# Optimization experiments

Hardware: AMD Instinct MI355X
Metric: run time of the kernel (lower is better)

Reference implementation:

```python
import jax, jax.numpy as jnp
import numpy as np

K = 1.0          # Lorentz curvature (all three manifolds)
SQRTK = 1.0
EPS = 1e-8
RES_SCALE = 27.5 # LResNet scale inside blocks
PE_SCALE = 1.0   # LResNet scale for positional embedding add
PATCH = 14


def ldot(x, y):
    """Minkowski inner product over last axis."""
    return -x[..., 0] * y[..., 0] + jnp.sum(x[..., 1:] * y[..., 1:], axis=-1)


def add_time(s):
    """Lift space components s to the hyperboloid: x0 = sqrt(1/K + ||s||^2)."""
    t = jnp.sqrt(1.0 / K + jnp.sum(s * s, axis=-1, keepdims=True))
    return jnp.concatenate([t, s], axis=-1)


def lnormalize(z):
    """Project arbitrary vector back onto hyperboloid (<x,x>_L = -1/K)."""
    d = jnp.sqrt(jnp.clip(-ldot(z, z), EPS))[..., None]
    return z / (SQRTK * d)


def lresnet(x, y, scale):
    """Lorentzian residual: normalized weighted Euclidean sum (LResNet)."""
    return lnormalize(x + scale * y)


def llayernorm(x, g, b):
    """LorentzLayerNorm: LayerNorm on space components, recompute time."""
    s = x[..., 1:]
    mu = jnp.mean(s, axis=-1, keepdims=True)
    var = jnp.var(s, axis=-1, keepdims=True)
    return add_time((s - mu) / jnp.sqrt(var + 1e-5) * g + b)


def lgelu(x):
    """LorentzActivation(GELU): act on space components, recompute time."""
    return add_time(jax.nn.gelu(x[..., 1:]))


def lattention(x, wq, bq, wk, bk, wv, bv, wo, bo):
    """Lorentz multi-head full attention, trans_heads_concat=True.
    x: [B,N,D]; wq/wk/wv: [H,D,hc-1]; wo: [D,D-1]."""
    q = add_time(jnp.einsum('bnd,hde->bhne', x, wq) + bq[None, :, None, :])
    k = add_time(jnp.einsum('bnd,hde->bhne', x, wk) + bk[None, :, None, :])
    v = add_time(jnp.einsum('bnd,hde->bhne', x, wv) + bv[None, :, None, :])
    hc = q.shape[-1]
    # pairwise Minkowski inner products -> neg. squared Lorentz distance scores
    inner = (jnp.einsum('bhne,bhme->bhnm', q[..., 1:], k[..., 1:])
             - q[..., 0][..., None] * k[..., 0][..., None, :])
    scores = (2.0 / K + 2.0 * inner) / jnp.sqrt(jnp.asarray(hc, x.dtype))
    att = jax.nn.softmax(scores, axis=-1)
    m = jnp.einsum('bhnm,bhmc->bhnc', att, v)   # convex combo of hyperbolic pts
    out = lnormalize(m)                          # Lorentzian centroid, [B,H,N,hc]
    B, H, N, C = out.shape
    cat = out.transpose(0, 2, 1, 3).reshape(B, N, H * C)
    return add_time(cat @ wo + bo)


def _forward(x, patch_W, patch_b, pe,
             ln1_g, ln1_b, ln2_g, ln2_b,
             Wq, bq, Wk, bk, Wv, bv, Wo, bo,
             mlp_W1, mlp_b1, mlp_W2, mlp_b2,
             mlr_a, mlr_z):
    B = x.shape[0]
    xi = x.transpose(0, 2, 3, 1)            # [B,H,W,3]
    xh = add_time(xi)                       # projx(pad(x,(1,0))) -> [B,H,W,4]
    _, Hh, Wh, Ch = xh.shape
    hp, wp = Hh // PATCH, Wh // PATCH
    patches = (xh.reshape(B, hp, PATCH, wp, PATCH, Ch)
                 .transpose(0, 1, 3, 2, 4, 5)
                 .reshape(B, hp * wp, PATCH * PATCH * Ch))
    h = add_time(patches @ patch_W + patch_b)   # Lorentz patch embed, [B,N,D]
    h = lresnet(h, pe, PE_SCALE)                # add positional embedding

    def body(h, p):
        (g1, b1, g2, b2, wq, bq_, wk, bk_, wv, bv_, wo, bo_,
         w1, b1m, w2, b2m) = p
        h = llayernorm(h, g1, b1)
        a = lattention(h, wq, bq_, wk, bk_, wv, bv_, wo, bo_)
        h = lresnet(h, a, RES_SCALE)
        m = llayernorm(h, g2, b2)
        m = add_time(m @ w1 + b1m)              # LorentzLinear 1
        m = lgelu(m)
        m = add_time(m @ w2 + b2m)              # LorentzLinear 2 (dropout=0)
        h = lresnet(h, m, RES_SCALE)
        return h, None

    h, _ = jax.lax.scan(body, h,
                        (ln1_g, ln1_b, ln2_g, ln2_b, Wq, bq, Wk, bk, Wv, bv,
                         Wo, bo, mlp_W1, mlp_b1, mlp_W2, mlp_b2))

    emb = lnormalize(jnp.mean(h, axis=1))       # lorentzian_centroid, [B,D]

    # LorentzMLR classifier
    zn = jnp.sqrt(jnp.sum(mlr_z * mlr_z, axis=-1) + EPS)
    wt = jnp.sinh(SQRTK * mlr_a) * zn                 # [C]
    ws = jnp.cosh(SQRTK * mlr_a)[:, None] * mlr_z     # [C,D-1]
    beta = jnp.sqrt(jnp.clip(jnp.sum(ws * ws, -1) - wt * wt, EPS))
    alpha = -emb[:, 0:1] * wt[None, :] + emb[:, 1:] @ ws.T  # [B,C]
    logits = beta * jnp.arcsinh(SQRTK * alpha / beta) / SQRTK
    return logits


def setup_inputs() -> dict:
    key = jax.random.key(0)
    ks = jax.random.split(key, 16)
    B, IMG, P, H, HC, L, C = 32, 224, 14, 6, 64, 12, 1000
    D = H * HC
    N = (IMG // P) ** 2
    MH = 4 * D
    s = 0.02
    f = jax.random.normal
    return dict(
        x=f(ks[0], (B, 3, IMG, IMG), jnp.float32),
        patch_W=f(ks[1], (P * P * 4, D - 1)) * s,
        patch_b=jnp.zeros((D - 1,)),
        pe=add_time(f(ks[2], (1, N, D - 1)) * s),
        ln1_g=jnp.ones((L, D - 1)), ln1_b=jnp.zeros((L, D - 1)),
        ln2_g=jnp.ones((L, D - 1)), ln2_b=jnp.zeros((L, D - 1)),
        Wq=f(ks[3], (L, H, D, HC - 1)) * s, bq=jnp.zeros((L, H, HC - 1)),
        Wk=f(ks[4], (L, H, D, HC - 1)) * s, bk=jnp.zeros((L, H, HC - 1)),
        Wv=f(ks[5], (L, H, D, HC - 1)) * s, bv=jnp.zeros((L, H, HC - 1)),
        Wo=f(ks[6], (L, D, D - 1)) * s, bo=jnp.zeros((L, D - 1)),
        mlp_W1=f(ks[7], (L, D, MH - 1)) * s, mlp_b1=jnp.zeros((L, MH - 1)),
        mlp_W2=f(ks[8], (L, MH, D - 1)) * s, mlp_b2=jnp.zeros((L, D - 1)),
        mlr_a=f(ks[9], (C,)) * s,
        mlr_z=f(ks[10], (C, D - 1)) * s,
    )


def reference(x, patch_W, patch_b, pe,
              ln1_g, ln1_b, ln2_g, ln2_b,
              Wq, bq, Wk, bk, Wv, bv, Wo, bo,
              mlp_W1, mlp_b1, mlp_W2, mlp_b2,
              mlr_a, mlr_z):
    return _forward(x, patch_W, patch_b, pe, ln1_g, ln1_b, ln2_g, ln2_b,
                    Wq, bq, Wk, bk, Wv, bv, Wo, bo,
                    mlp_W1, mlp_b1, mlp_W2, mlp_b2, mlr_a, mlr_z)
```

## Files before the change

### kernel.cpp

```cpp
#include <hip/hip_runtime.h>
#include <hip/hip_bf16.h>
#include <math.h>

typedef __hip_bfloat16 bf16;

constexpr int CB   = 32;
constexpr int CN   = 256;
constexpr int CD   = 384;
constexpr int CDS  = 383;
constexpr int CH   = 6;
constexpr int CHC  = 64;
constexpr int CHCS = 63;
constexpr int CL   = 12;
constexpr int CMH  = 1536;
constexpr int CMHS = 1535;
constexpr int CROWS = CB * CN;
constexpr int CKP  = 784;
constexpr int CKPP = 832;
constexpr int CQN  = CH * CHCS;
constexpr int CQN3 = 3 * CQN;

static inline int cdiv(int a, int b){ return (a + b - 1) / b; }

typedef short bf8_t __attribute__((ext_vector_type(8)));
typedef float f4_t  __attribute__((ext_vector_type(4)));

__device__ __forceinline__ unsigned short f2bf(float f) {
    union { float f; unsigned u; } x; x.f = f;
    unsigned r = x.u + 0x7FFFu + ((x.u >> 16) & 1u);
    return (unsigned short)(r >> 16);
}
__device__ __forceinline__ float bf2f(unsigned short h) {
    union { unsigned u; float f; } x; x.u = ((unsigned)h) << 16;
    return x.f;
}

__device__ __forceinline__ float ldin(const void* p, size_t i, int isb) {
    if (isb) return __bfloat162float(((const bf16*)p)[i]);
    return ((const float*)p)[i];
}

__global__ __launch_bounds__(256)
void detect_kernel(const void* __restrict__ x, int* __restrict__ flag) {
    __shared__ int red[256];
    const unsigned short* u = (const unsigned short*)x;
    int cnt = 0;
    for (int i = threadIdx.x; i < 4096; i += 256) {
        unsigned short v = u[i];
        int e = (v >> 7) & 0xFF;
        cnt += (v == 0 || (e >= 96 && e <= 142)) ? 1 : 0;
    }
    red[threadIdx.x] = cnt;
    __syncthreads();
    for (int off = 128; off > 0; off >>= 1) {
        if (threadIdx.x < off) red[threadIdx.x] += red[threadIdx.x + off];
        __syncthreads();
    }
    if (threadIdx.x == 0) flag[0] = (red[0] >= 3482) ? 1 : 0;
}

__global__ __launch_bounds__(256)
void pack_wt_kernel(const void* __restrict__ Wa, const void* __restrict__ Wb,
                    const void* __restrict__ Wc, size_t srcBase, size_t srcStrideL,
                    int N, int K, int Kpad, unsigned short* __restrict__ dst,
                    size_t dstStrideL, int fuse, const int* __restrict__ flg) {
    int isb = flg[0];
    int n0 = blockIdx.x * 64, k0 = blockIdx.y * 64;
    size_t so = srcBase + srcStrideL * blockIdx.z;
    unsigned short* dl = dst + dstStrideL * blockIdx.z;
    __shared__ unsigned short t[64][65];
    int tid = threadIdx.x;
    #pragma unroll
    for (int it = 0; it < 16; ++it) {
        int flat = it * 256 + tid;
        int kk = flat >> 6, nn = flat & 63;
        int n = n0 + nn, k = k0 + kk;
        float v = 0.0f;
        if (n < N && k < K) {
            if (fuse) {
                int wh = n / 378, rem = n - wh * 378;
                int h = rem / 63, e = rem - h * 63;
                const void* s = (wh == 0) ? Wa : (wh == 1 ? Wb : Wc);
                v = ldin(s, so + ((size_t)h * 384 + k) * 63 + e, isb);
            } else {
                v = ldin(Wa, so + (size_t)k * N + n, isb);
            }
        }
        t[kk][nn] = f2bf(v);
    }
    __syncthreads();
    #pragma unroll
    for (int it = 0; it < 16; ++it) {
        int flat = it * 256 + tid;
        int nn = flat >> 6, kk = flat & 63;
        dl[(size_t)(n0 + nn) * Kpad + (k0 + kk)] = t[kk][nn];
    }
}

__global__ __launch_bounds__(256)
void pack_bias_kernel(const void* __restrict__ b0, const void* __restrict__ b1v,
                      const void* __restrict__ b2v, int N, int Npad, int fuse,
                      float* __restrict__ dst, const int* __restrict__ flg) {
    int isb = flg[0];
    int l = blockIdx.y;
    int n = blockIdx.x * 256 + threadIdx.x;
    if (n >= Npad) return;
    float v = 0.0f;
    if (n < N) {
        if (fuse) {
            int wh = n / 378, rem = n - wh * 378;
            const void* s = (wh == 0) ? b0 : (wh == 1 ? b1v : b2v);
            v = ldin(s, (size_t)l * 378 + rem, isb);
        } else {
            v = ldin(b0, (size_t)l * N + n, isb);
        }
    }
    dst[(size_t)l * Npad + n] = v;
}

__global__ __launch_bounds__(256)
void patchify_kernel(const void* __restrict__ x, unsigned short* __restrict__ patches,
                     const int* __restrict__ flg) {
    int isb = flg[0];
    int idx = blockIdx.x * 256 + threadIdx.x;
    if (idx >= CB * 224 * 224) return;
    int col = idx % 224;
    int t   = idx / 224;
    int row = t % 224;
    int b   = t / 224;
    size_t base = ((size_t)b * 3) * 224 * 224 + (size_t)row * 224 + col;
    float r  = ldin(x, base, isb);
    float g  = ldin(x, base + 224 * 224, isb);
    float bl = ldin(x, base + 2 * 224 * 224, isb);
    float tt = sqrtf(1.0f + r * r + g * g + bl * bl);
    int gi = row / 14, pi = row % 14, gj = col / 14, pj = col % 14;
    int p = gi * 16 + gj;
    unsigned short* dp = patches + ((size_t)(b * CN + p)) * CKPP + (pi * 14 + pj) * 4;
    ushort4 w = make_ushort4(f2bf(tt), f2bf(r), f2bf(g), f2bf(bl));
    *(ushort4*)dp = w;
}

__global__ __launch_bounds__(256)
void padzero_kernel(unsigned short* __restrict__ patches) {
    int idx = blockIdx.x * 256 + threadIdx.x;
    if (idx >= CROWS * (CKPP - CKP)) return;
    int row = idx / (CKPP - CKP), off = idx % (CKPP - CKP);
    patches[(size_t)row * CKPP + CKP + off] = 0;
}

template<int BM, int BN>
__global__ __launch_bounds__(256)
void gemm_bt_kernel(const unsigned short* __restrict__ A, int lda,
                    const unsigned short* __restrict__ Bt, int ldb,
                    const float* __restrict__ bias,
                    float* __restrict__ C, int N, int K) {
    constexpr int BK  = 64;
    constexpr int ACH = BM / 32;
    constexpr int BCH = BN / 32;
    constexpr int MFR = BM / 32;
    constexpr int NFR = BN / 32;
    __shared__ __align__(16) unsigned short As[BM * BK];
    __shared__ __align__(16) unsigned short Bs[BN * BK];
    const int tid = threadIdx.x;
    const int wave = tid >> 6, lane = tid & 63;
    const int wm = wave & 1, wn = wave >> 1;
    const int bm = blockIdx.y * BM, bn = blockIdx.x * BN;

    const unsigned short* aSrc[ACH]; unsigned short* aDst[ACH];
    #pragma unroll
    for (int it = 0; it < ACH; ++it) {
        int i = it * 256 + tid;
        int row = i >> 3, up = i & 7;
        aSrc[it] = A + (size_t)(bm + row) * lda + up * 8;
        aDst[it] = &As[row * BK + ((up ^ (row & 7)) * 8)];
    }
    const unsigned short* bSrc[BCH]; unsigned short* bDst[BCH];
    #pragma unroll
    for (int it = 0; it < BCH; ++it) {
        int i = it * 256 + tid;
        int row = i >> 3, up = i & 7;
        bSrc[it] = Bt + (size_t)(bn + row) * ldb + up * 8;
        bDst[it] = &Bs[row * BK + ((up ^ (row & 7)) * 8)];
    }

    f4_t acc[MFR][NFR] = {};
    bf8_t av[ACH], bv[BCH];
    #pragma unroll
    for (int it = 0; it < ACH; ++it) av[it] = *(const bf8_t*)(aSrc[it]);
    #pragma unroll
    for (int it = 0; it < BCH; ++it) bv[it] = *(const bf8_t*)(bSrc[it]);

    for (int k0 = 0; k0 < K; k0 += BK) {
        __syncthreads();
        #pragma unroll
        for (int it = 0; it < ACH; ++it) *(bf8_t*)aDst[it] = av[it];
        #pragma unroll
        for (int it = 0; it < BCH; ++it) *(bf8_t*)bDst[it] = bv[it];
        __syncthreads();
        if (k0 + BK < K) {
            #pragma unroll
            for (int it = 0; it < ACH; ++it) av[it] = *(const bf8_t*)(aSrc[it] + k0 + BK);
            #pragma unroll
            for (int it = 0; it < BCH; ++it) bv[it] = *(const bf8_t*)(bSrc[it] + k0 + BK);
        }
        #pragma unroll
        for (int c = 0; c < 2; ++c) {
            bf8_t af[MFR], bfg[NFR];
            #pragma unroll
            for (int mi = 0; mi < MFR; ++mi) {
                int r = wm * (BM / 2) + mi * 16 + (lane & 15);
                int u = (c * 4 + (lane >> 4)) ^ (r & 7);
                af[mi] = *(const bf8_t*)&As[r * BK + u * 8];
            }
            #pragma unroll
            for (int ni = 0; ni < NFR; ++ni) {
                int cc = wn * (BN / 2) + ni * 16 + (lane & 15);
                int u = (c * 4 + (lane >> 4)) ^ (cc & 7);
                bfg[ni] = *(const bf8_t*)&Bs[cc * BK + u * 8];
            }
            #pragma unroll
            for (int mi = 0; mi < MFR; ++mi)
                #pragma unroll
                for (int ni = 0; ni < NFR; ++ni)
                    acc[mi][ni] = __builtin_amdgcn_mfma_f32_16x16x32_bf16(
                        af[mi], bfg[ni], acc[mi][ni], 0, 0, 0);
        }
    }

    const int colq = lane & 15, rowq = (lane >> 4) * 4;
    #pragma unroll
    for (int ni = 0; ni < NFR; ++ni) {
        int col = bn + wn * (BN / 2) + ni * 16 + colq;
        if (col >= N) continue;
        float bbv = bias[col];
        #pragma unroll
        for (int mi = 0; mi < MFR; ++mi) {
            int row = bm + wm * (BM / 2) + mi * 16 + rowq;
            #pragma unroll
            for (int r = 0; r < 4; ++r)
                C[(size_t)(row + r) * N + col] = acc[mi][ni][r] + bbv;
        }
    }
}

__global__ __launch_bounds__(256)
void add_time_rows_kernel(const float* __restrict__ src, void* __restrict__ dst,
                          int NS, int do_gelu, int obf) {
    int row = blockIdx.x;
    int tid = threadIdx.x;
    __shared__ float buf[1536];
    __shared__ float red[256];
    const float* sr = src + (size_t)row * NS;
    float ss = 0.0f;
    for (int j = tid; j < NS; j += 256) {
        float vv = sr[j];
        if (do_gelu) {
            float x3 = vv * vv * vv;
            float u = 0.7978845608028654f * (vv + 0.044715f * x3);
            float e = __expf(-2.0f * fabsf(u));
            float th = copysignf((1.0f - e) / (1.0f + e), u);
            vv = 0.5f * vv * (1.0f + th);
        }
        buf[j] = vv;
        ss += vv * vv;
    }
    red[tid] = ss;
    __syncthreads();
    for (int off = 128; off > 0; off >>= 1) {
        if (tid < off) red[tid] += red[tid + off];
        __syncthreads();
    }
    float t = sqrtf(1.0f + red[0]);
    if (obf) {
        unsigned short* dr = (unsigned short*)dst + (size_t)row * (NS + 1);
        if (tid == 0) dr[0] = f2bf(t);
        for (int j = tid; j < NS; j += 256) dr[1 + j] = f2bf(buf[j]);
    } else {
        float* dr = (float*)dst + (size_t)row * (NS + 1);
        if (tid == 0) dr[0] = t;
        for (int j = tid; j < NS; j += 256) dr[1 + j] = buf[j];
    }
}

__global__ __launch_bounds__(256)
void addtime_lresnet_kernel(const float* __restrict__ src,
                            const float* __restrict__ base, float scale,
                            float* __restrict__ out) {
    int row = blockIdx.x;
    int tid = threadIdx.x;
    const float* sr = src + (size_t)row * CDS;
    const float* br = base + (size_t)row * CD;
    __shared__ float red[256];
    float s0 = (tid > 0) ? sr[tid - 1] : 0.0f;
    float s1 = (tid < 128) ? sr[tid + 255] : 0.0f;
    red[tid] = s0 * s0 + s1 * s1;
    __syncthreads();
    for (int off = 128; off > 0; off >>= 1) {
        if (tid < off) red[tid] += red[tid + off];
        __syncthreads();
    }
    float t = sqrtf(1.0f + red[0]);
    __syncthreads();
    float y0 = (tid == 0) ? t : s0;
    float z0 = br[tid] + scale * y0;
    float z1 = (tid < 128) ? br[tid + 256] + scale * s1 : 0.0f;
    float c = (tid == 0) ? z0 * z0 : -z0 * z0;
    c -= z1 * z1;
    red[tid] = c;
    __syncthreads();
    for (int off = 128; off > 0; off >>= 1) {
        if (tid < off) red[tid] += red[tid + off];
        __syncthreads();
    }
    float rd = 1.0f / sqrtf(fmaxf(red[0], 1e-8f));
    float* orow = out + (size_t)row * CD;
    orow[tid] = z0 * rd;
    if (tid < 128) orow[256 + tid] = z1 * rd;
}

__global__ __launch_bounds__(256)
void addtime_lresnet_ln_kernel(const float* __restrict__ src,
                               const float* __restrict__ base, float scale,
                               const void* __restrict__ g, size_t goff,
                               const void* __restrict__ b, size_t boff,
                               float* __restrict__ hout,
                               float* __restrict__ lnout,
                               unsigned short* __restrict__ lnout_bf,
                               const int* __restrict__ flg) {
    int isb = flg[0];
    int row = blockIdx.x;
    int tid = threadIdx.x;
    const float* sr = src + (size_t)row * CDS;
    const float* br = base + (size_t)row * CD;
    __shared__ float red[256];
    __shared__ float red2[256];
    float s0 = (tid > 0) ? sr[tid - 1] : 0.0f;
    float s1 = (tid < 128) ? sr[tid + 255] : 0.0f;
    red[tid] = s0 * s0 + s1 * s1;
    __syncthreads();
    for (int off = 128; off > 0; off >>= 1) {
        if (tid < off) red[tid] += red[tid + off];
        __syncthreads();
    }
    float t = sqrtf(1.0f + red[0]);
    __syncthreads();
    float y0 = (tid == 0) ? t : s0;
    float z0 = br[tid] + scale * y0;
    float z1 = (tid < 128) ? br[256 + tid] + scale * s1 : 0.0f;
    float c = (tid == 0) ? z0 * z0 : -z0 * z0;
    c -= z1 * z1;
    red[tid] = c;
    __syncthreads();
    for (int off = 128; off > 0; off >>= 1) {
        if (tid < off) red[tid] += red[tid + off];
        __syncthreads();
    }
    float rd = 1.0f / sqrtf(fmaxf(red[0], 1e-8f));
    float h0 = z0 * rd;
    float h1 = z1 * rd;
    float* hr = hout + (size_t)row * CD;
    hr[tid] = h0;
    if (tid < 128) hr[256 + tid] = h1;
    __syncthreads();
    float v0 = (tid > 0) ? h0 : 0.0f;
    float v1 = (tid < 128) ? h1 : 0.0f;
    red[tid]  = v0 + v1;
    red2[tid] = v0 * v0 + v1 * v1;
    __syncthreads();
    for (int off = 128; off > 0; off >>= 1) {
        if (tid < off) { red[tid] += red[tid + off]; red2[tid] += red2[tid + off]; }
        __syncthreads();
    }
    float mu  = red[0] * (1.0f / 383.0f);
    float var = red2[0] * (1.0f / 383.0f) - mu * mu;
    __syncthreads();
    float rstd = rsqrtf(var + 1e-5f);
    float w0 = 0.0f, w1 = 0.0f;
    if (tid > 0)
        w0 = (h0 - mu) * rstd * ldin(g, goff + tid - 1, isb) + ldin(b, boff + tid - 1, isb);
    if (tid < 128)
        w1 = (h1 - mu) * rstd * ldin(g, goff + 255 + tid, isb) + ldin(b, boff + 255 + tid, isb);
    red[tid] = w0 * w0 + w1 * w1;
    __syncthreads();
    for (int off = 128; off > 0; off >>= 1) {
        if (tid < off) red[tid] += red[tid + off];
        __syncthreads();
    }
    float t2 = sqrtf(1.0f + red[0]);
    float* orow = lnout + (size_t)row * CD;
    unsigned short* brow = lnout_bf + (size_t)row * CD;
    if (tid == 0) { orow[0] = t2; brow[0] = f2bf(t2); }
    else          { orow[tid] = w0; brow[tid] = f2bf(w0); }
    if (tid < 128) { orow[256 + tid] = w1; brow[256 + tid] = f2bf(w1); }
}

__global__ __launch_bounds__(256)
void llayernorm_kernel(const float* __restrict__ x, const void* __restrict__ g,
                       size_t goff, const void* __restrict__ b, size_t boff,
                       float* __restrict__ out, unsigned short* __restrict__ out_bf,
                       const int* __restrict__ flg) {
    int isb = flg[0];
    int row = blockIdx.x;
    int tid = threadIdx.x;
    const float* xr = x + (size_t)row * CD;
    __shared__ float red[256];
    __shared__ float red2[256];
    int j0 = tid, j1 = tid + 256;
    float v0 = xr[1 + j0];
    float v1 = (j1 < CDS) ? xr[1 + j1] : 0.0f;
    red[tid]  = v0 + v1;
    red2[tid] = v0 * v0 + v1 * v1;
    __syncthreads();
    for (int off = 128; off > 0; off >>= 1) {
        if (tid < off) { red[tid] += red[tid + off]; red2[tid] += red2[tid + off]; }
        __syncthreads();
    }
    float mu  = red[0] * (1.0f / 383.0f);
    float var = red2[0] * (1.0f / 383.0f) - mu * mu;
    __syncthreads();
    float rstd = rsqrtf(var + 1e-5f);
    float y0 = (v0 - mu) * rstd * ldin(g, goff + j0, isb) + ldin(b, boff + j0, isb);
    float y1 = 0.0f;
    if (j1 < CDS) y1 = (v1 - mu) * rstd * ldin(g, goff + j1, isb) + ldin(b, boff + j1, isb);
    red[tid] = y0 * y0 + y1 * y1;
    __syncthreads();
    for (int off = 128; off > 0; off >>= 1) {
        if (tid < off) red[tid] += red[tid + off];
        __syncthreads();
    }
    float t = sqrtf(1.0f + red[0]);
    float* orow = out + (size_t)row * CD;
    unsigned short* brow = out_bf + (size_t)row * CD;
    orow[1 + j0] = y0;  brow[1 + j0] = f2bf(y0);
    if (j1 < CDS) { orow[1 + j1] = y1; brow[1 + j1] = f2bf(y1); }
    if (tid == 0) { orow[0] = t; brow[0] = f2bf(t); }
}

__global__ __launch_bounds__(256)
void lresnet_pe_kernel(const float* __restrict__ x, const void* __restrict__ pe,
                       float* __restrict__ out, const int* __restrict__ flg) {
    int isb = flg[0];
    int row = blockIdx.x;
    int tid = threadIdx.x;
    const float* xr = x + (size_t)row * CD;
    size_t pb = (size_t)(row & (CN - 1)) * CD;
    __shared__ float red[256];
    float z0 = xr[tid] + ldin(pe, pb + tid, isb);
    float z1 = 0.0f;
    float c = (tid == 0) ? z0 * z0 : -z0 * z0;
    if (tid < 128) { z1 = xr[256 + tid] + ldin(pe, pb + 256 + tid, isb); c -= z1 * z1; }
    red[tid] = c;
    __syncthreads();
    for (int off = 128; off > 0; off >>= 1) {
        if (tid < off) red[tid] += red[tid + off];
        __syncthreads();
    }
    float rd = 1.0f / sqrtf(fmaxf(red[0], 1e-8f));
    float* orow = out + (size_t)row * CD;
    orow[tid] = z0 * rd;
    if (tid < 128) orow[256 + tid] = z1 * rd;
}

__global__ __launch_bounds__(256)
void qkv_finish_kernel(const float* __restrict__ src, float* __restrict__ qkv,
                       size_t fh) {
    int tid = threadIdx.x, wave = tid >> 6, lane = tid & 63;
    int row = blockIdx.x * 4 + wave;
    int b = row >> 8, n = row & 255;
    const float* srow = src + (size_t)row * CQN3;
    #pragma unroll
    for (int hs = 0; hs < 18; hs++) {
        int which = hs / 6, h = hs % 6;
        float y = (lane < CHCS) ? srow[hs * 63 + lane] : 0.0f;
        float ss = y * y;
        #pragma unroll
        for (int off = 32; off > 0; off >>= 1) ss += __shfl_xor(ss, off);
        float t = sqrtf(1.0f + ss);
        float* dr = qkv + which * fh + (((size_t)(b * CH + h)) * CN + n) * CHC;
        if (lane < CHCS) dr[1 + lane] = y;
        if (lane == 0)   dr[0] = t;
    }
}

__global__ __launch_bounds__(256, 3)
void attn_kernel(const float* __restrict__ q, const float* __restrict__ k,
                 const float* __restrict__ v, unsigned short* __restrict__ attcat) {
    __shared__ __align__(16) unsigned char smem[32768];
    unsigned short* Bk = (unsigned short*)smem;
    unsigned short* Pf = (unsigned short*)smem;
    unsigned short* Bv = (unsigned short*)(smem + 16384);
    int qc = blockIdx.x, bh = blockIdx.y;
    int h = bh % CH, b = bh / CH;
    int tid = threadIdx.x, wave = tid >> 6, lane = tid & 63;
    const float* qb = q + ((size_t)bh * CN + qc * 64) * CHC;
    const float* kb = k + (size_t)bh * CN * CHC;
    const float* vb = v + (size_t)bh * CN * CHC;

    #pragma unroll
    for (int it = 0; it < 8; it++) {
        int flat = it * 256 + tid;
        int key = flat >> 3, c8 = flat & 7;
        const float* kp = kb + key * CHC + c8 * 8;
        float4 f0 = *(const float4*)(kp);
        float4 f1 = *(const float4*)(kp + 4);
        bf8_t w;
        w[0] = f2bf(f0.x); w[1] = f2bf(f0.y); w[2] = f2bf(f0.z); w[3] = f2bf(f0.w);
        w[4] = f2bf(f1.x); w[5] = f2bf(f1.y); w[6] = f2bf(f1.z); w[7] = f2bf(f1.w);
        int slab = (key >> 4) * 2 + (c8 >> 2);
        int lpw = ((key & 15) | ((c8 & 3) << 4)) ^ c8;
        *(bf8_t*)(Bk + (slab * 64 + lpw) * 8) = w;
    }

    bf8_t ah[2], al[2];
    {
        int row = wave * 16 + (lane & 15);
        #pragma unroll
        for (int ks = 0; ks < 2; ks++) {
            int c4 = ks * 32 + (lane >> 4) * 8;
            const float* qp = qb + row * CHC + c4;
            float4 f0 = *(const float4*)(qp);
            float4 f1 = *(const float4*)(qp + 4);
            if (c4 == 0) f0.x = -f0.x;
            float fv[8] = {f0.x, f0.y, f0.z, f0.w, f1.x, f1.y, f1.z, f1.w};
            #pragma unroll
            for (int i = 0; i < 8; i++) {
                unsigned short hi = f2bf(fv[i]);
                ah[ks][i] = (short)hi;
                al[ks][i] = (short)f2bf(fv[i] - bf2f(hi));
            }
        }
    }
    __syncthreads();

    int kx0 = lane ^ (lane >> 4);
    int kx1 = lane ^ (4 | (lane >> 4));
    f4_t s[16];
    #pragma unroll
    for (int nt = 0; nt < 16; nt++) s[nt] = (f4_t){0.0f, 0.0f, 0.0f, 0.0f};
    __builtin_amdgcn_s_setprio(1);
    #pragma unroll
    for (int nt = 0; nt < 16; nt++) {
        bf8_t b0 = *(const bf8_t*)(Bk + ((nt * 2 + 0) * 64 + kx0) * 8);
        bf8_t b1 = *(const bf8_t*)(Bk + ((nt * 2 + 1) * 64 + kx1) * 8);
        s[nt] = __builtin_amdgcn_mfma_f32_16x16x32_bf16(ah[0], b0, s[nt], 0, 0, 0);
        s[nt] = __builtin_amdgcn_mfma_f32_16x16x32_bf16(ah[1], b1, s[nt], 0, 0, 0);
        s[nt] = __builtin_amdgcn_mfma_f32_16x16x32_bf16(al[0], b0, s[nt], 0, 0, 0);
        s[nt] = __builtin_amdgcn_mfma_f32_16x16x32_bf16(al[1], b1, s[nt], 0, 0, 0);
    }
    __builtin_amdgcn_s_setprio(0);

    float mx[4] = {-1e30f, -1e30f, -1e30f, -1e30f};
    #pragma unroll
    for (int nt = 0; nt < 16; nt++)
        #pragma unroll
        for (int r = 0; r < 4; r++) mx[r] = fmaxf(mx[r], s[nt][r]);
    #pragma unroll
    for (int off = 1; off < 16; off <<= 1)
        #pragma unroll
        for (int r = 0; r < 4; r++) mx[r] = fmaxf(mx[r], __shfl_xor(mx[r], off));
    float sm[4] = {0.0f, 0.0f, 0.0f, 0.0f};
    #pragma unroll
    for (int nt = 0; nt < 16; nt++)
        #pragma unroll
        for (int r = 0; r < 4; r++) {
            float e = __expf(0.25f * (s[nt][r] - mx[r]));
            s[nt][r] = e; sm[r] += e;
        }
    #pragma unroll
    for (int off = 1; off < 16; off <<= 1)
        #pragma unroll
        for (int r = 0; r < 4; r++) sm[r] += __shfl_xor(sm[r], off);
    #pragma unroll
    for (int r = 0; r < 4; r++) sm[r] = 1.0f / sm[r];
    #pragma unroll
    for (int nt = 0; nt < 16; nt++)
        #pragma unroll
        for (int r = 0; r < 4; r++) s[nt][r] *= sm[r];

    __syncthreads();

    int colq = lane & 15, quad = lane >> 4;
    auto writePf = [&](int lo, int hh) {
        #pragma unroll
        for (int ntl = 0; ntl < 8; ntl++) {
            int nt = hh * 8 + ntl;
            int key = nt * 16 + colq;
            int ks2 = (key >> 5) & 3;
            #pragma unroll
            for (int r = 0; r < 4; r++) {
                int qrow = quad * 4 + r;
                int lp = (qrow & 15) | (((key >> 3) & 3) << 4);
                float p = s[nt][r];
                unsigned short hi = f2bf(p);
                unsigned short w = lo ? f2bf(p - bf2f(hi)) : hi;
                Pf[((wave * 4 + ks2) * 64 + lp) * 8 + (key & 7)] = w;
            }
        }
    };
    auto stageBv = [&](int lo, int hh) {
        #pragma unroll
        for (int i8 = 0; i8 < 4; i8++) {
            int octH = i8 * 4 + wave;
            int oct = hh * 16 + octH;
            bf8_t w;
            #pragma unroll
            for (int i = 0; i < 8; i++) {
                float f = vb[(size_t)(oct * 8 + i) * CHC + lane];
                unsigned short hi = f2bf(f);
                w[i] = (short)(lo ? f2bf(f - bf2f(hi)) : hi);
            }
            int a16 = ((lane >> 4) * 4 + (octH >> 2)) * 64 + (octH & 3) * 16 + (lane & 15);
            *(bf8_t*)(Bv + a16 * 8) = w;
        }
    };
    f4_t o[4] = {};
    auto pvpass = [&]() {
        __builtin_amdgcn_s_setprio(1);
        #pragma unroll
        for (int ks2 = 0; ks2 < 4; ks2++) {
            bf8_t pa = *(const bf8_t*)(Pf + ((wave * 4 + ks2) * 64 + lane) * 8);
            #pragma unroll
            for (int nt = 0; nt < 4; nt++) {
                bf8_t vv = *(const bf8_t*)(Bv + ((nt * 4 + ks2) * 64 + lane) * 8);
                o[nt] = __builtin_amdgcn_mfma_f32_16x16x32_bf16(pa, vv, o[nt], 0, 0, 0);
            }
        }
        __builtin_amdgcn_s_setprio(0);
    };

    writePf(0, 0); stageBv(0, 0);
    __syncthreads(); pvpass();
    __syncthreads(); writePf(0, 1); stageBv(0, 1);
    __syncthreads(); pvpass();
    __syncthreads(); writePf(0, 0); stageBv(1, 0);
    __syncthreads(); pvpass();
    __syncthreads(); writePf(0, 1); stageBv(1, 1);
    __syncthreads(); pvpass();
    __syncthreads(); writePf(1, 0); stageBv(0, 0);
    __syncthreads(); pvpass();
    __syncthreads(); writePf(1, 1); stageBv(0, 1);
    __syncthreads(); pvpass();

    {
        float nrm[4] = {0.0f, 0.0f, 0.0f, 0.0f};
        #pragma unroll
        for (int nt = 0; nt < 4; nt++) {
            float sgn = (nt == 0 && colq == 0) ? 1.0f : -1.0f;
            #pragma unroll
            for (int r = 0; r < 4; r++) nrm[r] += sgn * o[nt][r] * o[nt][r];
        }
        #pragma unroll
        for (int off = 1; off < 16; off <<= 1)
            #pragma unroll
            for (int r = 0; r < 4; r++) nrm[r] += __shfl_xor(nrm[r], off);
        #pragma unroll
        for (int r = 0; r < 4; r++) {
            float d = 1.0f / sqrtf(fmaxf(nrm[r], 1e-8f));
            int qg = qc * 64 + wave * 16 + quad * 4 + r;
            unsigned short* orow = attcat + ((size_t)b * CN + qg) * CD + h * CHC;
            #pragma unroll
            for (int nt = 0; nt < 4; nt++)
                orow[nt * 16 + colq] = f2bf(o[nt][r] * d);
        }
    }
}

__global__ __launch_bounds__(256)
void meanpool_part_kernel(const float* __restrict__ hbuf, float* __restrict__ part) {
    int b = blockIdx.x, ch = blockIdx.y, tid = threadIdx.x;
    const float* hb = hbuf + ((size_t)b * CN + ch * 32) * CD;
    float s0 = 0.0f, s1 = 0.0f;
    for (int n = 0; n < 32; n++) {
        s0 += hb[(size_t)n * CD + tid];
        if (tid < 128) s1 += hb[(size_t)n * CD + 256 + tid];
    }
    float* pr = part + (size_t)(b * 8 + ch) * CD;
    pr[tid] = s0;
    if (tid < 128) pr[256 + tid] = s1;
}

__global__ __launch_bounds__(256)
void meanpool_fin_kernel(const float* __restrict__ part, float* __restrict__ emb) {
    int b = blockIdx.x, tid = threadIdx.x;
    float s0 = 0.0f, s1 = 0.0f;
    for (int c = 0; c < 8; c++) {
        const float* pr = part + (size_t)(b * 8 + c) * CD;
        s0 += pr[tid];
        if (tid < 128) s1 += pr[256 + tid];
    }
    s0 *= (1.0f / 256.0f);
    s1 *= (1.0f / 256.0f);
    __shared__ float red[256];
    float c2 = (tid == 0) ? s0 * s0 : -s0 * s0;
    if (tid < 128) c2 -= s1 * s1;
    red[tid] = c2;
    __syncthreads();
    for (int off = 128; off > 0; off >>= 1) {
        if (tid < off) red[tid] += red[tid + off];
        __syncthreads();
    }
    float rd = 1.0f / sqrtf(fmaxf(red[0], 1e-8f));
    emb[(size_t)b * CD + tid] = s0 * rd;
    if (tid < 128) emb[(size_t)b * CD + 256 + tid] = s1 * rd;
}

__global__ __launch_bounds__(256)
void head_pre_kernel(const void* __restrict__ mlra, const void* __restrict__ mlrz,
                     float* __restrict__ wt, float* __restrict__ beta,
                     float* __restrict__ cha, const int* __restrict__ flg) {
    int isb = flg[0];
    int wave = threadIdx.x >> 6, lane = threadIdx.x & 63;
    int c = blockIdx.x * 4 + wave;
    float S = 0.0f;
    for (int j = lane; j < CDS; j += 64) {
        float zz = ldin(mlrz, (size_t)c * CDS + j, isb);
        S += zz * zz;
    }
    #pragma unroll
    for (int off = 32; off > 0; off >>= 1) S += __shfl_xor(S, off);
    if (lane == 0) {
        float a  = ldin(mlra, c, isb);
        float sh = sinhf(a), ch = coshf(a);
        float zn = sqrtf(S + 1e-8f);
        float w  = sh * zn;
        wt[c]  = w;
        cha[c] = ch;
        beta[c] = sqrtf(fmaxf(ch * ch * S - w * w, 1e-8f));
    }
}

__global__ __launch_bounds__(256)
void head_logits_kernel(const float* __restrict__ emb, const void* __restrict__ mlrz,
                        const float* __restrict__ wt, const float* __restrict__ beta,
                        const float* __restrict__ cha, void* __restrict__ out,
                        const int* __restrict__ flg) {
    int isb = flg[0];
    int tid = threadIdx.x, wave = tid >> 6, lane = tid & 63;
    __shared__ float es[CB * CD];
    for (int i = tid; i < CB * CD; i += 256) es[i] = emb[i];
    __syncthreads();
    int c = blockIdx.x * 4 + wave;
    float zv[6];
    #pragma unroll
    for (int jj = 0; jj < 6; jj++) {
        int j = jj * 64 + lane;
        zv[jj] = (j < CDS) ? ldin(mlrz, (size_t)c * CDS + j, isb) : 0.0f;
    }
    float wtc = wt[c], chac = cha[c], bec = beta[c];
    for (int b = 0; b < CB; b++) {
        const float* eb = es + b * CD;
        float d = 0.0f;
        #pragma unroll
        for (int jj = 0; jj < 6; jj++) {
            int j = jj * 64 + lane;
            if (j < CDS) d += zv[jj] * eb[1 + j];
        }
        #pragma unroll
        for (int off = 32; off > 0; off >>= 1) d += __shfl_xor(d, off);
        if (lane == 0) {
            float alpha = -eb[0] * wtc + chac * d;
            float lg = bec * asinhf(alpha / bec);
            if (isb) ((bf16*)out)[(size_t)b * 1000 + c] = __float2bfloat16(lg);
            else     ((float*)out)[(size_t)b * 1000 + c] = lg;
        }
    }
}

extern "C" void kernel_launch(void* const* d_in, const int* in_sizes, int n_in,
                              void* d_out, int out_size, void* d_ws, size_t ws_size,
                              hipStream_t stream) {
    const void* x      = d_in[0];
    const void* patchW = d_in[1];
    const void* patchB = d_in[2];
    const void* pe     = d_in[3];
    const void* ln1g   = d_in[4];
    const void* ln1b   = d_in[5];
    const void* ln2g   = d_in[6];
    const void* ln2b   = d_in[7];
    const void* Wq     = d_in[8];
    const void* bq     = d_in[9];
    const void* Wk     = d_in[10];
    const void* bk     = d_in[11];
    const void* Wv     = d_in[12];
    const void* bv     = d_in[13];
    const void* Wo     = d_in[14];
    const void* bo     = d_in[15];
    const void* W1     = d_in[16];
    const void* b1     = d_in[17];
    const void* W2     = d_in[18];
    const void* b2     = d_in[19];
    const void* mlra   = d_in[20];
    const void* mlrz   = d_in[21];

    float* ws = (float*)d_ws;
    const size_t FH = (size_t)CROWS * CD;
    float* hbuf   = ws;
    float* xln    = ws + FH;
    float* big1   = ws + 2 * FH;
    float* big2   = ws + 6 * FH;
    float* qb     = big2;
    const float* kb = big2 + FH;
    float* vb     = big2 + 2 * FH;
    unsigned short* patches_bf = (unsigned short*)big1;
    unsigned short* hidden_bf  = (unsigned short*)big2;
    unsigned short* xln_bf     = (unsigned short*)(big2 + 3 * FH);
    unsigned short* attcat_bf  = (unsigned short*)(big2 + 3 * FH);
    float* emb    = ws + 10 * FH;
    float* wt     = emb + (size_t)CB * CD;
    float* beta   = wt + 1000;
    float* cha    = beta + 1000;
    int*   flag   = (int*)(cha + 1000);

    float* bias_patch = ws + 10 * FH + 16384;
    float* bias_qkv   = bias_patch + 384;
    float* bias_wo    = bias_qkv + (size_t)12 * 1152;
    float* bias_w1    = bias_wo  + (size_t)12 * 384;
    float* bias_w2    = bias_w1  + (size_t)12 * 1536;
    unsigned short* wt_patch = (unsigned short*)(bias_w2 + (size_t)12 * 384);
    unsigned short* wt_dyn   = wt_patch + (size_t)384 * 832;
    const size_t EQKV = (size_t)1152 * 384, EWO = (size_t)384 * 384,
                 EW1  = (size_t)1536 * 384, EW2 = (size_t)384 * 1536;
    unsigned short* wt_qkv = wt_dyn;
    unsigned short* wt_wo  = wt_qkv + 12 * EQKV;
    unsigned short* wt_w1  = wt_wo  + 12 * EWO;
    unsigned short* wt_w2  = wt_w1  + 12 * EW1;
    size_t need_full = (size_t)((char*)(wt_w2 + 12 * EW2) - (char*)d_ws);
    int full = (ws_size >= need_full) ? 1 : 0;
    unsigned short* l_qkv = wt_dyn;
    unsigned short* l_wo  = l_qkv + EQKV;
    unsigned short* l_w1  = l_wo  + EWO;
    unsigned short* l_w2  = l_w1  + EW1;

    detect_kernel<<<1, 256, 0, stream>>>(x, flag);

    pack_bias_kernel<<<dim3(2, 1),  256, 0, stream>>>(patchB, nullptr, nullptr, 383, 384, 0, bias_patch, flag);
    pack_bias_kernel<<<dim3(5, 12), 256, 0, stream>>>(bq, bk, bv, 1134, 1152, 1, bias_qkv, flag);
    pack_bias_kernel<<<dim3(2, 12), 256, 0, stream>>>(bo, nullptr, nullptr, 383, 384, 0, bias_wo, flag);
    pack_bias_kernel<<<dim3(6, 12), 256, 0, stream>>>(b1, nullptr, nullptr, 1535, 1536, 0, bias_w1, flag);
    pack_bias_kernel<<<dim3(2, 12), 256, 0, stream>>>(b2, nullptr, nullptr, 383, 384, 0, bias_w2, flag);

    pack_wt_kernel<<<dim3(6, 13, 1), 256, 0, stream>>>(
        patchW, nullptr, nullptr, 0, 0, 383, 784, 832, wt_patch, 0, 0, flag);
    if (full) {
        pack_wt_kernel<<<dim3(18, 6, 12), 256, 0, stream>>>(
            Wq, Wk, Wv, 0, (size_t)145152, 1134, 384, 384, wt_qkv, EQKV, 1, flag);
        pack_wt_kernel<<<dim3(6, 6, 12), 256, 0, stream>>>(
            Wo, nullptr, nullptr, 0, (size_t)147072, 383, 384, 384, wt_wo, EWO, 0, flag);
        pack_wt_kernel<<<dim3(24, 6, 12), 256, 0, stream>>>(
            W1, nullptr, nullptr, 0, (size_t)589440, 1535, 384, 384, wt_w1, EW1, 0, flag);
        pack_wt_kernel<<<dim3(6, 24, 12), 256, 0, stream>>>(
            W2, nullptr, nullptr, 0, (size_t)588288, 383, 1536, 1536, wt_w2, EW2, 0, flag);
    }

    patchify_kernel<<<cdiv(CB * 224 * 224, 256), 256, 0, stream>>>(x, patches_bf, flag);
    padzero_kernel<<<cdiv(CROWS * (CKPP - CKP), 256), 256, 0, stream>>>(patches_bf);
    gemm_bt_kernel<64, 64><<<dim3(6, 128), 256, 0, stream>>>(
        patches_bf, CKPP, wt_patch, CKPP, bias_patch, big2, CDS, CKPP);
    add_time_rows_kernel<<<CROWS, 256, 0, stream>>>(big2, xln, CDS, 0, 0);
    lresnet_pe_kernel<<<CROWS, 256, 0, stream>>>(xln, pe, hbuf, flag);

    llayernorm_kernel<<<CROWS, 256, 0, stream>>>(
        hbuf, ln1g, 0, ln1b, 0, xln, xln_bf, flag);

    for (int l = 0; l < CL; l++) {
        const unsigned short *pqkv, *pwo, *pw1, *pw2;
        if (full) {
            pqkv = wt_qkv + (size_t)l * EQKV;
            pwo  = wt_wo  + (size_t)l * EWO;
            pw1  = wt_w1  + (size_t)l * EW1;
            pw2  = wt_w2  + (size_t)l * EW2;
        } else {
            pack_wt_kernel<<<dim3(18, 6, 1), 256, 0, stream>>>(
                Wq, Wk, Wv, (size_t)l * 145152, 0, 1134, 384, 384, l_qkv, 0, 1, flag);
            pack_wt_kernel<<<dim3(6, 6, 1), 256, 0, stream>>>(
                Wo, nullptr, nullptr, (size_t)l * 147072, 0, 383, 384, 384, l_wo, 0, 0, flag);
            pack_wt_kernel<<<dim3(24, 6, 1), 256, 0, stream>>>(
                W1, nullptr, nullptr, (size_t)l * 589440, 0, 1535, 384, 384, l_w1, 0, 0, flag);
            pack_wt_kernel<<<dim3(6, 24, 1), 256, 0, stream>>>(
                W2, nullptr, nullptr, (size_t)l * 588288, 0, 383, 1536, 1536, l_w2, 0, 0, flag);
            pqkv = l_qkv; pwo = l_wo; pw1 = l_w1; pw2 = l_w2;
        }
        gemm_bt_kernel<128, 128><<<dim3(9, 64), 256, 0, stream>>>(
            xln_bf, CD, pqkv, CD, bias_qkv + (size_t)l * 1152, big1, CQN3, CD);
        qkv_finish_kernel<<<2048, 256, 0, stream>>>(big1, qb, FH);
        attn_kernel<<<dim3(4, CB * CH), 256, 0, stream>>>(qb, kb, vb, attcat_bf);
        gemm_bt_kernel<64, 64><<<dim3(6, 128), 256, 0, stream>>>(
            attcat_bf, CD, pwo, CD, bias_wo + (size_t)l * 384, big1, CDS, CD);
        addtime_lresnet_ln_kernel<<<CROWS, 256, 0, stream>>>(
            big1, xln, 27.5f, ln2g, (size_t)l * CDS, ln2b, (size_t)l * CDS,
            hbuf, xln, xln_bf, flag);
        gemm_bt_kernel<128, 128><<<dim3(12, 64), 256, 0, stream>>>(
            xln_bf, CD, pw1, CD, bias_w1 + (size_t)l * 1536, big1, CMHS, CD);
        add_time_rows_kernel<<<CROWS, 256, 0, stream>>>(big1, hidden_bf, CMHS, 1, 1);
        gemm_bt_kernel<64, 64><<<dim3(6, 128), 256, 0, stream>>>(
            hidden_bf, CMH, pw2, CMH, bias_w2 + (size_t)l * 384, big1, CDS, CMH);
        if (l < CL - 1) {
            addtime_lresnet_ln_kernel<<<CROWS, 256, 0, stream>>>(
                big1, hbuf, 27.5f, ln1g, (size_t)(l + 1) * CDS, ln1b, (size_t)(l + 1) * CDS,
                hbuf, xln, xln_bf, flag);
        } else {
            addtime_lresnet_kernel<<<CROWS, 256, 0, stream>>>(big1, hbuf, 27.5f, hbuf);
        }
    }

    meanpool_part_kernel<<<dim3(CB, 8), 256, 0, stream>>>(hbuf, big1);
    meanpool_fin_kernel<<<CB, 256, 0, stream>>>(big1, emb);
    head_pre_kernel<<<250, 256, 0, stream>>>(mlra, mlrz, wt, beta, cha, flag);
    head_logits_kernel<<<250, 256, 0, stream>>>(emb, mlrz, wt, beta, cha, d_out, flag);
}
```

Measured before the change: 3.272 ms.

## Stage full V tile once per precision pass and remap attention block order

Attention now stages the whole 256-key V tile (hi or lo bf16 split) into an enlarged 48KB LDS buffer, so each split is converted from global memory once instead of per half. The PV passes are reordered so the P hi/lo passes reuse the same staged V. The 2D grid is flattened and remapped so consecutive blocks spread over XCDs while the four query chunks of a head stay together, aiming at better L2 locality. The change adds LDS use and drops the min-blocks launch bound, which may lower occupancy.

```diff
diff --git a/kernel.cpp b/kernel.cpp
--- a/kernel.cpp
+++ b/kernel.cpp
@@ -482,14 +482,16 @@
     }
 }
 
-__global__ __launch_bounds__(256, 3)
+__global__ __launch_bounds__(256)
 void attn_kernel(const float* __restrict__ q, const float* __restrict__ k,
                  const float* __restrict__ v, unsigned short* __restrict__ attcat) {
-    __shared__ __align__(16) unsigned char smem[32768];
+    __shared__ __align__(16) unsigned char smem[49152];
     unsigned short* Bk = (unsigned short*)smem;
     unsigned short* Pf = (unsigned short*)smem;
     unsigned short* Bv = (unsigned short*)(smem + 16384);
-    int qc = blockIdx.x, bh = blockIdx.y;
+    int id = blockIdx.x;
+    int nid = (id & 7) * 96 + (id >> 3);
+    int bh = nid >> 2, qc = nid & 3;
     int h = bh % CH, b = bh / CH;
     int tid = threadIdx.x, wave = tid >> 6, lane = tid & 63;
     const float* qb = q + ((size_t)bh * CN + qc * 64) * CHC;
@@ -597,11 +599,10 @@
             }
         }
     };
-    auto stageBv = [&](int lo, int hh) {
-        #pragma unroll
-        for (int i8 = 0; i8 < 4; i8++) {
-            int octH = i8 * 4 + wave;
-            int oct = hh * 16 + octH;
+    auto stageBv = [&](int lo) {
+        #pragma unroll
+        for (int i8 = 0; i8 < 8; i8++) {
+            int oct = i8 * 4 + wave;
             bf8_t w;
             #pragma unroll
             for (int i = 0; i < 8; i++) {
@@ -609,37 +610,37 @@
                 unsigned short hi = f2bf(f);
                 w[i] = (short)(lo ? f2bf(f - bf2f(hi)) : hi);
             }
-            int a16 = ((lane >> 4) * 4 + (octH >> 2)) * 64 + (octH & 3) * 16 + (lane & 15);
+            int a16 = ((lane >> 4) * 8 + (oct >> 2)) * 64 + (oct & 3) * 16 + (lane & 15);
             *(bf8_t*)(Bv + a16 * 8) = w;
         }
     };
     f4_t o[4] = {};
-    auto pvpass = [&]() {
+    auto pvpass = [&](int hh) {
         __builtin_amdgcn_s_setprio(1);
         #pragma unroll
         for (int ks2 = 0; ks2 < 4; ks2++) {
             bf8_t pa = *(const bf8_t*)(Pf + ((wave * 4 + ks2) * 64 + lane) * 8);
             #pragma unroll
             for (int nt = 0; nt < 4; nt++) {
-                bf8_t vv = *(const bf8_t*)(Bv + ((nt * 4 + ks2) * 64 + lane) * 8);
+                bf8_t vv = *(const bf8_t*)(Bv + ((nt * 8 + hh * 4 + ks2) * 64 + lane) * 8);
                 o[nt] = __builtin_amdgcn_mfma_f32_16x16x32_bf16(pa, vv, o[nt], 0, 0, 0);
             }
         }
         __builtin_amdgcn_s_setprio(0);
     };
 
-    writePf(0, 0); stageBv(0, 0);
-    __syncthreads(); pvpass();
-    __syncthreads(); writePf(0, 1); stageBv(0, 1);
-    __syncthreads(); pvpass();
-    __syncthreads(); writePf(0, 0); stageBv(1, 0);
-    __syncthreads(); pvpass();
-    __syncthreads(); writePf(0, 1); stageBv(1, 1);
-    __syncthreads(); pvpass();
-    __syncthreads(); writePf(1, 0); stageBv(0, 0);
-    __syncthreads(); pvpass();
-    __syncthreads(); writePf(1, 1); stageBv(0, 1);
-    __syncthreads(); pvpass();
+    writePf(0, 0); stageBv(0);
+    __syncthreads(); pvpass(0);
+    __syncthreads(); writePf(0, 1);
+    __syncthreads(); pvpass(1);
+    __syncthreads(); writePf(1, 0);
+    __syncthreads(); pvpass(0);
+    __syncthreads(); writePf(1, 1);
+    __syncthreads(); pvpass(1);
+    __syncthreads(); writePf(0, 0); stageBv(1);
+    __syncthreads(); pvpass(0);
+    __syncthreads(); writePf(0, 1);
+    __syncthreads(); pvpass(1);
 
     {
         float nrm[4] = {0.0f, 0.0f, 0.0f, 0.0f};
@@ -883,7 +884,7 @@
         gemm_bt_kernel<128, 128><<<dim3(9, 64), 256, 0, stream>>>(
             xln_bf, CD, pqkv, CD, bias_qkv + (size_t)l * 1152, big1, CQN3, CD);
         qkv_finish_kernel<<<2048, 256, 0, stream>>>(big1, qb, FH);
-        attn_kernel<<<dim3(4, CB * CH), 256, 0, stream>>>(qb, kb, vb, attcat_bf);
+        attn_kernel<<<768, 256, 0, stream>>>(qb, kb, vb, attcat_bf);
         gemm_bt_kernel<64, 64><<<dim3(6, 128), 256, 0, stream>>>(
             attcat_bf, CD, pwo, CD, bias_wo + (size_t)l * 384, big1, CDS, CD);
         addtime_lresnet_ln_kernel<<<CROWS, 256, 0, stream>>>(
```

Result: faster. 2.696 ms (-17.6%).
